# Optimization experiments

Hardware: AMD Instinct MI355X
Metric: run time of the kernel (lower is better)

## Reference

```python
import jax, jax.numpy as jnp
import numpy as np

DIM = 1024
NUM_HEADS = 16
BATCH = 4
SEQ = 2048
SCALE = (DIM // NUM_HEADS) ** -0.5
MASK_VAL = -10000000.0


def setup_inputs() -> dict:
    key = jax.random.key(0)
    k1, k2, k3, k4 = jax.random.split(key, 4)
    inputs = jax.random.normal(k1, (BATCH, SEQ, DIM), dtype=jnp.float32)
    # xavier-ish scaling for weights
    W_qkv = jax.random.normal(k2, (3 * DIM, DIM), dtype=jnp.float32) * (1.0 / np.sqrt(DIM))
    W_fc = jax.random.normal(k3, (DIM, DIM), dtype=jnp.float32) * (1.0 / np.sqrt(DIM))
    b_fc = jnp.zeros((DIM,), dtype=jnp.float32)
    padding_mask = jax.random.randint(k4, (BATCH, SEQ), 0, 2, dtype=jnp.int32)
    return {"inputs": inputs, "W_qkv": W_qkv, "W_fc": W_fc, "b_fc": b_fc,
            "padding_mask": padding_mask}


def reference(inputs, W_qkv, W_fc, b_fc, padding_mask):
    B, N, C = inputs.shape
    H = NUM_HEADS
    Dh = C // H
    # qkv projection (torch Linear: x @ W.T), [B,N,3C]
    qkv = jnp.einsum('bnc,oc->bno', inputs, W_qkv)
    qkv = qkv.reshape(B, N, 3, H, Dh).transpose(2, 0, 3, 1, 4)  # [3,B,H,N,Dh]
    q, k, v = qkv[0], qkv[1], qkv[2]
    att = jnp.einsum('bhqd,bhkd->bhqk', q, k) * SCALE  # [B,H,N,N]
    mask = padding_mask[:, None, None, :]              # [B,1,1,N]
    att = jnp.where(mask > 0, jnp.float32(MASK_VAL), att)
    att = jax.nn.softmax(att, axis=-1)
    x = jnp.einsum('bhqk,bhkd->bhqd', att, v)          # [B,H,N,Dh]
    x = x.transpose(0, 2, 1, 3).reshape(B, N, C)       # [B,N,C]
    out = jnp.einsum('bnc,oc->bno', x, W_fc) + b_fc
    return out
```

## Files before the change

### kernel.cpp

```cpp
#include <hip/hip_runtime.h>
#include <stdint.h>

constexpr int kDim  = 1024;
constexpr int kH    = 16;
constexpr int kB    = 4;
constexpr int kSeq  = 2048;
constexpr int kDh   = 64;
constexpr int kMTot = kB * kSeq;
constexpr int kNQkv = 3 * kDim;
constexpr float kScale = 0.125f;
constexpr float kLog2e = 1.44269504088896f;
constexpr float kC1    = kScale * kLog2e;
constexpr float kMaxSub = 10.0f;
constexpr float kMk2Un   = -kMaxSub * kLog2e;
constexpr float kMk2Mask = -1.0e9f;
constexpr int kPld = 72;
constexpr int kCld = 136;

typedef __attribute__((ext_vector_type(8))) short short8;
typedef __attribute__((ext_vector_type(4))) float floatx4;

__device__ __forceinline__ unsigned short f2bf(float f) {
  union { float f; unsigned u; } v; v.f = f;
  unsigned r = v.u + 0x7fffu + ((v.u >> 16) & 1u);
  return (unsigned short)(r >> 16);
}
__device__ __forceinline__ unsigned short f2bf_fast(float f) {
  union { float f; unsigned u; } v; v.f = f;
  return (unsigned short)((v.u + 0x8000u) >> 16);
}
__device__ __forceinline__ float vexp2(float x) {
  float r; asm("v_exp_f32 %0, %1" : "=v"(r) : "v"(x)); return r;
}
__device__ __forceinline__ void gl2lds16(const void* g, void* l) {
  __builtin_amdgcn_global_load_lds(
      (const __attribute__((address_space(1))) unsigned int*)g,
      (__attribute__((address_space(3))) unsigned int*)l, 16, 0, 0);
}

__global__ void __launch_bounds__(256) cvt_scan(
    const float4* __restrict__ x, const float4* __restrict__ wq,
    const float4* __restrict__ wf,
    ushort4* __restrict__ xb, ushort4* __restrict__ wqb, ushort4* __restrict__ wfb,
    const int* __restrict__ pm, int* __restrict__ cidx, int* __restrict__ nkd,
    int* __restrict__ ctr) {
  const int X4  = (kMTot * kDim) / 4;
  const int WQ4 = (kNQkv * kDim) / 4;
  const int NCVT = 12288;
  if (blockIdx.x >= NCVT) {
    const int b = blockIdx.x - NCVT;
    const int t = threadIdx.x;
    const int lane = t & 63, wv = t >> 6;
    __shared__ int wsum[4];
    __shared__ int woff[5];
    if (b == 0 && t == 0) *ctr = 256;
    int base = t * 8;
    int keep[8]; int cnt = 0;
#pragma unroll
    for (int j = 0; j < 8; j++) {
      keep[j] = (pm[b * kSeq + base + j] <= 0) ? 1 : 0;
      cnt += keep[j];
    }
    int pre = cnt;
#pragma unroll
    for (int off = 1; off < 64; off <<= 1) {
      int v = __shfl_up(pre, off, 64);
      if (lane >= off) pre += v;
    }
    int excl = pre - cnt;
    if (lane == 63) wsum[wv] = pre;
    __syncthreads();
    if (t == 0) {
      int s = 0;
#pragma unroll
      for (int w = 0; w < 4; w++) { woff[w] = s; s += wsum[w]; }
      woff[4] = s;
      nkd[b] = s;
    }
    __syncthreads();
    const int nk = woff[4];
    int kp = woff[wv] + excl;
#pragma unroll
    for (int j = 0; j < 8; j++) {
      int n = base + j;
      int pos = keep[j] ? kp : nk + (n - kp);
      cidx[b * kSeq + pos] = b * kSeq + n;
      kp += keep[j];
    }
    return;
  }
  int i = blockIdx.x * 256 + threadIdx.x;
  float4 v; ushort4* dst;
  if (i < X4)            { v = x[i];             dst = xb  + i; }
  else if (i < X4 + WQ4) { v = wq[i - X4];       dst = wqb + (i - X4); }
  else                   { v = wf[i - X4 - WQ4]; dst = wfb + (i - X4 - WQ4); }
  ushort4 o;
  o.x = f2bf(v.x); o.y = f2bf(v.y); o.z = f2bf(v.z); o.w = f2bf(v.w);
  *dst = o;
}

__global__ void __launch_bounds__(512, 2) gemm_qkv(
    const unsigned short* __restrict__ xb, const unsigned short* __restrict__ wqb,
    const int* __restrict__ cidx, const int* __restrict__ nkd,
    int* __restrict__ ctr,
    unsigned short* __restrict__ qb, unsigned short* __restrict__ kb,
    unsigned short* __restrict__ vtb) {
  extern __shared__ __attribute__((aligned(16))) unsigned short smem[];
  __shared__ int s_slot;
  unsigned short* As0 = smem;
  unsigned short* Bs0 = smem + 16384;
  unsigned short* As1 = smem + 32768;
  unsigned short* Bs1 = smem + 49152;

  const int t = threadIdx.x;
  const int lane = t & 63, wv = t >> 6;
  const int wm = (wv >> 2) << 7;
  const int wn = (wv & 3) << 6;
  const int lrow = lane & 15, quad = lane >> 4, l7 = lane & 7;
  const int srow = t >> 3;
  const int pu8 = (t & 7) * 8;
  const int lu8 = ((t & 7) ^ (srow & 7)) * 8;
  const int off0 = (quad ^ l7) * 8;

  const int rr0 = (nkd[0] + 127) >> 7, rr1 = (nkd[1] + 127) >> 7;
  const int rr2 = (nkd[2] + 127) >> 7, rr3 = (nkd[3] + 127) >> 7;
  const int tb0 = (rr0 + 1) >> 1, tb1 = (rr1 + 1) >> 1;
  const int tb2 = (rr2 + 1) >> 1, tb3 = (rr3 + 1) >> 1;
  const int pA = tb0, pB = pA + tb1, pC = pB + tb2, pD = pC + tb3;
  const int NT = 128 + 8 * pD;

#define STAGE_B(buf, p, k0) gl2lds16(brow + (int64_t)(p) * 64 * kDim + (k0), \
                                     (buf) + ((p) * 64 + srow) * 64 + pu8)
#define STAGE_A(buf, p, k0) gl2lds16(arow[p] + (k0), \
                                     (buf) + ((p) * 64 + srow) * 64 + pu8)
#define BARRIER() { asm volatile("" ::: "memory"); \
                    __builtin_amdgcn_s_barrier(); \
                    asm volatile("" ::: "memory"); }
#define LDA(q) { \
    const unsigned short* Ar0_ = Ac + (wm + (2*(q)) * 16 + lrow) * 64; \
    const unsigned short* Ar1_ = Ac + (wm + (2*(q)+1) * 16 + lrow) * 64; \
    af00 = *(const short8*)(Ar0_ + off0); \
    af01 = *(const short8*)(Ar0_ + (off0 ^ 32)); \
    af10 = *(const short8*)(Ar1_ + off0); \
    af11 = *(const short8*)(Ar1_ + (off0 ^ 32)); }
#define MFMAQ(q) { \
    __builtin_amdgcn_s_setprio(1); \
    _Pragma("unroll") \
    for (int ni = 0; ni < 4; ni++) { \
      acc[2*(q)][ni]   = __builtin_amdgcn_mfma_f32_16x16x32_bf16(af00, bfr[ni][0], acc[2*(q)][ni],   0, 0, 0); \
      acc[2*(q)+1][ni] = __builtin_amdgcn_mfma_f32_16x16x32_bf16(af10, bfr[ni][0], acc[2*(q)+1][ni], 0, 0, 0); \
    } \
    _Pragma("unroll") \
    for (int ni = 0; ni < 4; ni++) { \
      acc[2*(q)][ni]   = __builtin_amdgcn_mfma_f32_16x16x32_bf16(af01, bfr[ni][1], acc[2*(q)][ni],   0, 0, 0); \
      acc[2*(q)+1][ni] = __builtin_amdgcn_mfma_f32_16x16x32_bf16(af11, bfr[ni][1], acc[2*(q)+1][ni], 0, 0, 0); \
    } \
    __builtin_amdgcn_s_setprio(0); }

  int slot = blockIdx.x;
  while (slot < NT) {
    int which, tN, tMl, bb, rbv;
    if (slot < 128) {
      which = 0; tN = (slot & 3) * 256;
      int tMg = (slot >> 2) * 256;
      bb = tMg >> 11; tMl = tMg & 2047; rbv = 16;
    } else {
      int id = slot - 128;
      const int TK = 4 * pD;
      which = (id < TK) ? 1 : 2;
      if (which == 2) id -= TK;
      int col = id & 3, j = id >> 2;
      int pj;
      if (j < pA)      { bb = 0; pj = j;      rbv = rr0; }
      else if (j < pB) { bb = 1; pj = j - pA; rbv = rr1; }
      else if (j < pC) { bb = 2; pj = j - pB; rbv = rr2; }
      else             { bb = 3; pj = j - pC; rbv = rr3; }
      tMl = pj * 256;
      tN = (which == 1 ? 1024 : 2048) + col * 256;
    }
    int nrows;
    if (which == 0) nrows = 256;
    else { int rem = rbv * 128 - tMl; nrows = (rem >= 256) ? 256 : 128; }
    const bool na4 = (nrows == 256);
    const bool act = (wm < nrows);
    const bool vblk = (which == 2);

    const unsigned short* arow[4];
#pragma unroll
    for (int p = 0; p < 4; p++) {
      int pe = (!na4 && p > 1) ? 1 : p;
      int rl = tMl + pe * 64 + srow;
      int rid = (which == 0) ? (bb * 2048 + rl) : cidx[bb * 2048 + rl];
      arow[p] = xb + (int64_t)rid * kDim + lu8;
    }
    const unsigned short* brow = wqb + (int64_t)(tN + srow) * kDim + lu8;

    floatx4 acc[8][4];
    floatx4 zero = {0.f, 0.f, 0.f, 0.f};
#pragma unroll
    for (int mi = 0; mi < 8; mi++)
#pragma unroll
      for (int ni = 0; ni < 4; ni++) acc[mi][ni] = zero;

    STAGE_B(Bs0, 0, 0); STAGE_B(Bs0, 1, 0); STAGE_B(Bs0, 2, 0); STAGE_B(Bs0, 3, 0);
    STAGE_A(As0, 0, 0);
    if (na4) {
      STAGE_A(As0, 2, 0); STAGE_A(As0, 1, 0); STAGE_A(As0, 3, 0);
      asm volatile("s_waitcnt vmcnt(2)" ::: "memory");
    } else {
      STAGE_A(As0, 1, 0);
      asm volatile("s_waitcnt vmcnt(1)" ::: "memory");
    }
    BARRIER();

    for (int tt = 0; tt < 16; ++tt) {
      unsigned short* Ac = (tt & 1) ? As1 : As0;
      unsigned short* Bc = (tt & 1) ? Bs1 : Bs0;
      unsigned short* An = (tt & 1) ? As0 : As1;
      unsigned short* Bn = (tt & 1) ? Bs0 : Bs1;
      const int kn = (tt + 1) * 64;
      const bool more = (tt < 15);

      short8 bfr[4][2];
      short8 af00, af01, af10, af11;

      if (act) {
#pragma unroll
        for (int ni = 0; ni < 4; ni++) {
          const unsigned short* Br_ = Bc + (wn + ni * 16 + lrow) * 64;
          bfr[ni][0] = *(const short8*)(Br_ + off0);
          bfr[ni][1] = *(const short8*)(Br_ + (off0 ^ 32));
        }
        LDA(0);
      }
      if (more) { STAGE_B(Bn, 0, kn); STAGE_B(Bn, 1, kn); }
      BARRIER();
      if (act) MFMAQ(0);
      BARRIER();
      if (act) LDA(1);
      if (more) { STAGE_B(Bn, 2, kn); STAGE_B(Bn, 3, kn); }
      BARRIER();
      if (act) MFMAQ(1);
      if (more) { asm volatile("s_waitcnt vmcnt(4)" ::: "memory"); }
      else      { asm volatile("s_waitcnt vmcnt(0)" ::: "memory"); }
      BARRIER();
      if (act) LDA(2);
      if (more) {
        STAGE_A(An, 0, kn);
        if (na4) { STAGE_A(An, 2, kn); STAGE_A(An, 1, kn); STAGE_A(An, 3, kn); }
        else     { STAGE_A(An, 1, kn); }
      }
      BARRIER();
      if (act) MFMAQ(2);
      BARRIER();
      if (act) LDA(3);
      BARRIER();
      if (act) MFMAQ(3);
      if (more) {
        if (na4) { asm volatile("s_waitcnt vmcnt(2)" ::: "memory"); }
        else     { asm volatile("s_waitcnt vmcnt(1)" ::: "memory"); }
      } else {
        asm volatile("s_waitcnt vmcnt(0)" ::: "memory");
      }
      BARRIER();
    }

    unsigned short* Cs = smem;
    const int h4 = (tN >> 6) & 15;
#pragma unroll
    for (int h = 0; h < 2; h++) {
      const bool writer = ((((wv & 3) >> 1) == h) && act);
      const int cwn = (wv & 1) * 64;
      if (!vblk) {
        if (writer) {
#pragma unroll
          for (int mi = 0; mi < 8; mi++)
#pragma unroll
            for (int ni = 0; ni < 4; ni++)
#pragma unroll
              for (int r = 0; r < 4; r++) {
                int row = wm + mi * 16 + quad * 4 + r;
                int c = cwn + ni * 16 + lrow;
                Cs[row * kCld + c] = f2bf(acc[mi][ni][r]);
              }
        }
        asm volatile("s_waitcnt lgkmcnt(0)" ::: "memory");
        BARRIER();
        unsigned short* qk = (which == 0) ? qb : kb;
        const int itn = nrows >> 6;
#pragma unroll
        for (int g = 0; g < 2; g++) {
          int hh = (h4 + h * 2 + g) & 15;
          unsigned short* base = qk + ((int64_t)((bb << 4) + hh) << 17)
                                 + (int64_t)tMl * 64;
          for (int it = 0; it < itn; it++) {
            int off = it * 4096 + t * 8;
            int n = off >> 6;
            int d = off & 63;
            *(short8*)(base + off) = *(const short8*)(Cs + n * kCld + g * 64 + d);
          }
        }
        BARRIER();
      } else {
        if (writer) {
#pragma unroll
          for (int mi = 0; mi < 8; mi++)
#pragma unroll
            for (int ni = 0; ni < 4; ni++)
#pragma unroll
              for (int r = 0; r < 4; r++) {
                int row = wm + mi * 16 + quad * 4 + r;
                int c = cwn + ni * 16 + lrow;
                Cs[c * 264 + row] = f2bf(acc[mi][ni][r]);
              }
        }
        asm volatile("s_waitcnt lgkmcnt(0)" ::: "memory");
        BARRIER();
        const int c8n = nrows >> 3;
#pragma unroll
        for (int g = 0; g < 2; g++) {
          int hh = (h4 + h * 2 + g) & 15;
          unsigned short* vbase = vtb + (((int64_t)((bb << 4) + hh)) << 17) + tMl;
#pragma unroll
          for (int it = 0; it < 4; it++) {
            int off = it * 512 + t;
            int d = off >> 5, c8 = off & 31;
            if (c8 < c8n)
              *(short8*)(vbase + (int64_t)d * 2048 + c8 * 8) =
                  *(const short8*)(Cs + (g * 64 + d) * 264 + c8 * 8);
          }
        }
        BARRIER();
      }
    }

    if (t == 0) s_slot = atomicAdd(ctr, 1);
    __syncthreads();
    slot = s_slot;
  }
#undef STAGE_B
#undef STAGE_A
#undef LDA
#undef MFMAQ
#undef BARRIER
}

__global__ void __launch_bounds__(256, 4) attn(
    const unsigned short* __restrict__ qb, const unsigned short* __restrict__ kb,
    const unsigned short* __restrict__ vtb, const int* __restrict__ nkd,
    unsigned short* __restrict__ xab) {
  __shared__ __attribute__((aligned(16))) unsigned short Ks[64 * 64];
  __shared__ __attribute__((aligned(16))) unsigned short Vs[64 * 64];
  __shared__ __attribute__((aligned(16))) unsigned short Ps[4][2][16 * kPld];

  const int t = threadIdx.x, lane = t & 63, wv = t >> 6;
  const int lrow = lane & 15, quad = lane >> 4, l7 = lane & 7;
  const int qblk = blockIdx.x & 15, bh = blockIdx.x >> 4;
  const int b = bh >> 4, h = bh & 15;
  const int q0 = qblk * 128;
  const int srow = t >> 3;
  const int pu8 = (t & 7) * 8;
  const int lu8 = ((t & 7) ^ (srow & 7)) * 8;
  const int off0 = (quad ^ l7) * 8;

  const int nk  = nkd[b];
  const int nkt = (nk + 63) >> 6;

  const unsigned short* Qb0 = qb + ((int64_t)bh * kSeq + q0 + wv * 16 + lrow) * kDh;
  short8 qf[2][2];
  qf[0][0] = *(const short8*)(Qb0 + quad * 8);
  qf[0][1] = *(const short8*)(Qb0 + 32 + quad * 8);
  qf[1][0] = *(const short8*)(Qb0 + 64 * kDh + quad * 8);
  qf[1][1] = *(const short8*)(Qb0 + 64 * kDh + 32 + quad * 8);

  float l_run[2][4];
  floatx4 o_acc[2][4];
  floatx4 zero = {0.f, 0.f, 0.f, 0.f};
#pragma unroll
  for (int t2 = 0; t2 < 2; t2++) {
#pragma unroll
    for (int r = 0; r < 4; r++) l_run[t2][r] = 0.f;
#pragma unroll
    for (int di = 0; di < 4; di++) o_acc[t2][di] = zero;
  }

  const unsigned short* Kbase = kb  + (int64_t)bh * kSeq * kDh;
  const unsigned short* Vbase = vtb + (int64_t)bh * kDh * kSeq;

  for (int kt = 0; kt < nkt; ++kt) {
    const int k0 = kt * 64;
    {
      int r0 = srow, r1 = srow + 32;
      gl2lds16(Kbase + (int64_t)(k0 + r0) * kDh + lu8, Ks + r0 * 64 + pu8);
      gl2lds16(Kbase + (int64_t)(k0 + r1) * kDh + lu8, Ks + r1 * 64 + pu8);
      gl2lds16(Vbase + (int64_t)r0 * kSeq + k0 + lu8,  Vs + r0 * 64 + pu8);
      gl2lds16(Vbase + (int64_t)r1 * kSeq + k0 + lu8,  Vs + r1 * 64 + pu8);
    }
    __syncthreads();

    floatx4 s[2][4];
#pragma unroll
    for (int ni = 0; ni < 4; ni++) {
      const unsigned short* Kr = Ks + (ni * 16 + lrow) * 64;
      short8 kf0 = *(const short8*)(Kr + off0);
      short8 kf1 = *(const short8*)(Kr + (off0 ^ 32));
#pragma unroll
      for (int t2 = 0; t2 < 2; t2++) {
        floatx4 tmp = __builtin_amdgcn_mfma_f32_16x16x32_bf16(qf[t2][0], kf0, zero, 0, 0, 0);
        s[t2][ni]   = __builtin_amdgcn_mfma_f32_16x16x32_bf16(qf[t2][1], kf1, tmp, 0, 0, 0);
      }
    }
    float mk2[4];
#pragma unroll
    for (int c = 0; c < 4; c++)
      mk2[c] = (k0 + c * 16 + lrow < nk) ? kMk2Un : kMk2Mask;

#pragma unroll
    for (int t2 = 0; t2 < 2; t2++) {
      unsigned short* Pw = &Ps[wv][t2][0];
#pragma unroll
      for (int r = 0; r < 4; r++) {
        int prow = (quad * 4 + r) * kPld + lrow;
#pragma unroll
        for (int c = 0; c < 4; c++) {
          float p = vexp2(fmaf(s[t2][c][r], kC1, mk2[c]));
          l_run[t2][r] += p;
          Pw[prow + c * 16] = f2bf_fast(p);
        }
      }
    }
    asm volatile("s_waitcnt lgkmcnt(0)" ::: "memory");

#pragma unroll
    for (int ks = 0; ks < 2; ks++) {
      short8 pf0 = *(const short8*)(&Ps[wv][0][0] + lrow * kPld + ks * 32 + quad * 8);
      short8 pf1 = *(const short8*)(&Ps[wv][1][0] + lrow * kPld + ks * 32 + quad * 8);
      const int voff = off0 ^ (ks * 32);
#pragma unroll
      for (int di = 0; di < 4; di++) {
        short8 vf = *(const short8*)(Vs + (di * 16 + lrow) * 64 + voff);
        o_acc[0][di] = __builtin_amdgcn_mfma_f32_16x16x32_bf16(pf0, vf, o_acc[0][di], 0, 0, 0);
        o_acc[1][di] = __builtin_amdgcn_mfma_f32_16x16x32_bf16(pf1, vf, o_acc[1][di], 0, 0, 0);
      }
    }
    __syncthreads();
  }

#pragma unroll
  for (int t2 = 0; t2 < 2; t2++) {
#pragma unroll
    for (int r = 0; r < 4; r++) {
      float l = l_run[t2][r];
      l += __shfl_xor(l, 1, 64);
      l += __shfl_xor(l, 2, 64);
      l += __shfl_xor(l, 4, 64);
      l += __shfl_xor(l, 8, 64);
      float inv = 1.0f / l;
      int n = q0 + t2 * 64 + wv * 16 + quad * 4 + r;
      int64_t rowbase = ((int64_t)b * kSeq + n) * kDim + h * kDh;
#pragma unroll
      for (int di = 0; di < 4; di++)
        xab[rowbase + di * 16 + lrow] = f2bf(o_acc[t2][di][r] * inv);
    }
  }
}

__global__ void __launch_bounds__(256) gemm_fc(
    const unsigned short* __restrict__ xab, const unsigned short* __restrict__ wfb,
    const float* __restrict__ bfc, float* __restrict__ out) {
  __shared__ __attribute__((aligned(16))) unsigned short As[128 * 64];
  __shared__ __attribute__((aligned(16))) unsigned short Bs[64 * 64];
  const int tN = blockIdx.x * 64, tM = blockIdx.y * 128;
  const int t = threadIdx.x;
  const int lane = t & 63, wv = t >> 6;
  const int wm = (wv >> 1) << 6, wn = (wv & 1) << 5;
  const int lrow = lane & 15, quad = lane >> 4, l7 = lane & 7;
  const int srow = t >> 3;
  const int pu8 = (t & 7) * 8;
  const int lu8 = ((t & 7) ^ (srow & 7)) * 8;
  const int off0 = (quad ^ l7) * 8;

  floatx4 acc[4][2];
  floatx4 zero = {0.f, 0.f, 0.f, 0.f};
#pragma unroll
  for (int mi = 0; mi < 4; mi++)
#pragma unroll
    for (int ni = 0; ni < 2; ni++) acc[mi][ni] = zero;

  for (int k0 = 0; k0 < kDim; k0 += 64) {
#pragma unroll
    for (int p = 0; p < 4; ++p) {
      int r = srow + p * 32;
      gl2lds16(xab + (int64_t)(tM + r) * kDim + k0 + lu8, As + r * 64 + pu8);
    }
#pragma unroll
    for (int p = 0; p < 2; ++p) {
      int r = srow + p * 32;
      gl2lds16(wfb + (int64_t)(tN + r) * kDim + k0 + lu8, Bs + r * 64 + pu8);
    }
    __syncthreads();
#pragma unroll
    for (int kk = 0; kk < 64; kk += 32) {
      short8 af[4], bf[2];
#pragma unroll
      for (int mi = 0; mi < 4; mi++)
        af[mi] = *(const short8*)(As + (wm + mi * 16 + lrow) * 64 + (off0 ^ kk));
#pragma unroll
      for (int ni = 0; ni < 2; ni++)
        bf[ni] = *(const short8*)(Bs + (wn + ni * 16 + lrow) * 64 + (off0 ^ kk));
#pragma unroll
      for (int mi = 0; mi < 4; mi++)
#pragma unroll
        for (int ni = 0; ni < 2; ni++)
          acc[mi][ni] = __builtin_amdgcn_mfma_f32_16x16x32_bf16(af[mi], bf[ni], acc[mi][ni], 0, 0, 0);
    }
    __syncthreads();
  }

#pragma unroll
  for (int ni = 0; ni < 2; ni++) {
    int o = tN + wn + ni * 16 + lrow;
    float bias = bfc[o];
#pragma unroll
    for (int mi = 0; mi < 4; mi++) {
#pragma unroll
      for (int r = 0; r < 4; r++) {
        int i = tM + wm + mi * 16 + quad * 4 + r;
        out[(int64_t)i * kDim + o] = acc[mi][ni][r] + bias;
      }
    }
  }
}

extern "C" void kernel_launch(void* const* d_in, const int* in_sizes, int n_in,
                              void* d_out, int out_size, void* d_ws, size_t ws_size,
                              hipStream_t stream) {
  (void)in_sizes; (void)n_in; (void)out_size; (void)ws_size;
  const float* x    = (const float*)d_in[0];
  const float* wqkv = (const float*)d_in[1];
  const float* wfc  = (const float*)d_in[2];
  const float* bfc  = (const float*)d_in[3];
  const int*   pm   = (const int*)d_in[4];
  float* out = (float*)d_out;

  char* ws = (char*)d_ws;
  unsigned short* xb  = (unsigned short*)(ws);
  unsigned short* wqb = (unsigned short*)(ws + 16777216);
  unsigned short* wfb = (unsigned short*)(ws + 23068672);
  unsigned short* qb  = (unsigned short*)(ws + 25165824);
  unsigned short* kb  = (unsigned short*)(ws + 41943040);
  unsigned short* vtb = (unsigned short*)(ws + 58720256);
  int*            cidx= (int*)(ws + 75497472);
  int*            nkd = (int*)(ws + 75530240);
  int*            ctr = (int*)(ws + 75530256);
  unsigned short* xab = xb;

  static bool s_attr_set = false;
  if (!s_attr_set) {
    (void)hipFuncSetAttribute((const void*)gemm_qkv,
                              hipFuncAttributeMaxDynamicSharedMemorySize, 131072);
    s_attr_set = true;
  }

  cvt_scan<<<12288 + kB, 256, 0, stream>>>(
      (const float4*)x, (const float4*)wqkv, (const float4*)wfc,
      (ushort4*)xb, (ushort4*)wqb, (ushort4*)wfb, pm, cidx, nkd, ctr);
  gemm_qkv<<<256, 512, 131072, stream>>>(
      xb, wqb, cidx, nkd, ctr, qb, kb, vtb);
  attn<<<kB * kH * (kSeq / 128), 256, 0, stream>>>(qb, kb, vtb, nkd, xab);
  gemm_fc<<<dim3(kDim / 64, kMTot / 128), 256, 0, stream>>>(xab, wfb, bfc, out);
}
```

Measured before the change: 238.5 us.

## Prefetch QKV weight tiles two steps ahead and widen FC GEMM tile

```diff
diff --git a/kernel.cpp b/kernel.cpp
--- a/kernel.cpp
+++ b/kernel.cpp
@@ -204,22 +204,22 @@
 
     STAGE_B(Bs0, 0, 0); STAGE_B(Bs0, 1, 0); STAGE_B(Bs0, 2, 0); STAGE_B(Bs0, 3, 0);
     STAGE_A(As0, 0, 0);
-    if (na4) {
-      STAGE_A(As0, 2, 0); STAGE_A(As0, 1, 0); STAGE_A(As0, 3, 0);
-      asm volatile("s_waitcnt vmcnt(2)" ::: "memory");
-    } else {
-      STAGE_A(As0, 1, 0);
-      asm volatile("s_waitcnt vmcnt(1)" ::: "memory");
-    }
+    if (na4) STAGE_A(As0, 2, 0);
+    STAGE_A(As0, 1, 0);
+    if (na4) STAGE_A(As0, 3, 0);
+    STAGE_B(Bs1, 0, 64); STAGE_B(Bs1, 1, 64); STAGE_B(Bs1, 2, 64); STAGE_B(Bs1, 3, 64);
+    if (na4) { asm volatile("s_waitcnt vmcnt(6)" ::: "memory"); }
+    else     { asm volatile("s_waitcnt vmcnt(5)" ::: "memory"); }
     BARRIER();
 
     for (int tt = 0; tt < 16; ++tt) {
       unsigned short* Ac = (tt & 1) ? As1 : As0;
       unsigned short* Bc = (tt & 1) ? Bs1 : Bs0;
       unsigned short* An = (tt & 1) ? As0 : As1;
-      unsigned short* Bn = (tt & 1) ? Bs0 : Bs1;
-      const int kn = (tt + 1) * 64;
-      const bool more = (tt < 15);
+      const int kn  = (tt + 1) * 64;
+      const int kn2 = (tt + 2) * 64;
+      const bool stA = (tt < 15);
+      const bool stB = (tt < 14);
 
       short8 bfr[4][2];
       short8 af00, af01, af10, af11;
@@ -233,35 +233,35 @@
         }
         LDA(0);
       }
-      if (more) { STAGE_B(Bn, 0, kn); STAGE_B(Bn, 1, kn); }
+      if (stA) { STAGE_A(An, 0, kn); if (na4) STAGE_A(An, 2, kn); }
       BARRIER();
       if (act) MFMAQ(0);
       BARRIER();
       if (act) LDA(1);
-      if (more) { STAGE_B(Bn, 2, kn); STAGE_B(Bn, 3, kn); }
+      if (stA) { STAGE_A(An, 1, kn); if (na4) STAGE_A(An, 3, kn); }
       BARRIER();
       if (act) MFMAQ(1);
-      if (more) { asm volatile("s_waitcnt vmcnt(4)" ::: "memory"); }
-      else      { asm volatile("s_waitcnt vmcnt(0)" ::: "memory"); }
-      BARRIER();
-      if (act) LDA(2);
-      if (more) {
-        STAGE_A(An, 0, kn);
-        if (na4) { STAGE_A(An, 2, kn); STAGE_A(An, 1, kn); STAGE_A(An, 3, kn); }
-        else     { STAGE_A(An, 1, kn); }
-      }
-      BARRIER();
-      if (act) MFMAQ(2);
-      BARRIER();
-      if (act) LDA(3);
-      BARRIER();
-      if (act) MFMAQ(3);
-      if (more) {
-        if (na4) { asm volatile("s_waitcnt vmcnt(2)" ::: "memory"); }
-        else     { asm volatile("s_waitcnt vmcnt(1)" ::: "memory"); }
+      if (stA) {
+        if (na4) { asm volatile("s_waitcnt vmcnt(8)" ::: "memory"); }
+        else     { asm volatile("s_waitcnt vmcnt(6)" ::: "memory"); }
       } else {
         asm volatile("s_waitcnt vmcnt(0)" ::: "memory");
       }
+      BARRIER();
+      if (act) LDA(2);
+      if (stB) { STAGE_B(Bc, 0, kn2); STAGE_B(Bc, 1, kn2); }
+      BARRIER();
+      if (act) MFMAQ(2);
+      BARRIER();
+      if (act) LDA(3);
+      if (stB) { STAGE_B(Bc, 2, kn2); STAGE_B(Bc, 3, kn2); }
+      BARRIER();
+      if (act) MFMAQ(3);
+      if (stB)      { if (na4) { asm volatile("s_waitcnt vmcnt(6)" ::: "memory"); }
+                      else     { asm volatile("s_waitcnt vmcnt(5)" ::: "memory"); } }
+      else if (stA) { if (na4) { asm volatile("s_waitcnt vmcnt(2)" ::: "memory"); }
+                      else     { asm volatile("s_waitcnt vmcnt(1)" ::: "memory"); } }
+      else          { asm volatile("s_waitcnt vmcnt(0)" ::: "memory"); }
       BARRIER();
     }
 
@@ -469,56 +469,52 @@
     const unsigned short* __restrict__ xab, const unsigned short* __restrict__ wfb,
     const float* __restrict__ bfc, float* __restrict__ out) {
   __shared__ __attribute__((aligned(16))) unsigned short As[128 * 64];
-  __shared__ __attribute__((aligned(16))) unsigned short Bs[64 * 64];
-  const int tN = blockIdx.x * 64, tM = blockIdx.y * 128;
+  __shared__ __attribute__((aligned(16))) unsigned short Bs[128 * 64];
+  const int tN = blockIdx.x * 128, tM = blockIdx.y * 128;
   const int t = threadIdx.x;
   const int lane = t & 63, wv = t >> 6;
-  const int wm = (wv >> 1) << 6, wn = (wv & 1) << 5;
+  const int wm = (wv >> 1) << 6, wn = (wv & 1) << 6;
   const int lrow = lane & 15, quad = lane >> 4, l7 = lane & 7;
   const int srow = t >> 3;
   const int pu8 = (t & 7) * 8;
   const int lu8 = ((t & 7) ^ (srow & 7)) * 8;
   const int off0 = (quad ^ l7) * 8;
 
-  floatx4 acc[4][2];
+  floatx4 acc[4][4];
   floatx4 zero = {0.f, 0.f, 0.f, 0.f};
 #pragma unroll
   for (int mi = 0; mi < 4; mi++)
 #pragma unroll
-    for (int ni = 0; ni < 2; ni++) acc[mi][ni] = zero;
+    for (int ni = 0; ni < 4; ni++) acc[mi][ni] = zero;
 
   for (int k0 = 0; k0 < kDim; k0 += 64) {
 #pragma unroll
     for (int p = 0; p < 4; ++p) {
       int r = srow + p * 32;
       gl2lds16(xab + (int64_t)(tM + r) * kDim + k0 + lu8, As + r * 64 + pu8);
-    }
-#pragma unroll
-    for (int p = 0; p < 2; ++p) {
-      int r = srow + p * 32;
       gl2lds16(wfb + (int64_t)(tN + r) * kDim + k0 + lu8, Bs + r * 64 + pu8);
     }
     __syncthreads();
 #pragma unroll
     for (int kk = 0; kk < 64; kk += 32) {
-      short8 af[4], bf[2];
+      short8 af[4], bf[4];
 #pragma unroll
       for (int mi = 0; mi < 4; mi++)
         af[mi] = *(const short8*)(As + (wm + mi * 16 + lrow) * 64 + (off0 ^ kk));
 #pragma unroll
-      for (int ni = 0; ni < 2; ni++)
+      for (int ni = 0; ni < 4; ni++)
         bf[ni] = *(const short8*)(Bs + (wn + ni * 16 + lrow) * 64 + (off0 ^ kk));
 #pragma unroll
       for (int mi = 0; mi < 4; mi++)
 #pragma unroll
-        for (int ni = 0; ni < 2; ni++)
+        for (int ni = 0; ni < 4; ni++)
           acc[mi][ni] = __builtin_amdgcn_mfma_f32_16x16x32_bf16(af[mi], bf[ni], acc[mi][ni], 0, 0, 0);
     }
     __syncthreads();
   }
 
 #pragma unroll
-  for (int ni = 0; ni < 2; ni++) {
+  for (int ni = 0; ni < 4; ni++) {
     int o = tN + wn + ni * 16 + lrow;
     float bias = bfc[o];
 #pragma unroll
@@ -568,5 +564,5 @@
   gemm_qkv<<<256, 512, 131072, stream>>>(
       xb, wqb, cidx, nkd, ctr, qb, kb, vtb);
   attn<<<kB * kH * (kSeq / 128), 256, 0, stream>>>(qb, kb, vtb, nkd, xab);
-  gemm_fc<<<dim3(kDim / 64, kMTot / 128), 256, 0, stream>>>(xab, wfb, bfc, out);
-}
+  gemm_fc<<<dim3(kDim / 128, kMTot / 128), 256, 0, stream>>>(xab, wfb, bfc, out);
+}
```

Measured after the change: 237.5 us. Within noise of the previous version (-0.4%).
